# Optimization experiments

Measured on AMD Instinct MI355X. Metric: run time of the kernel, lower is better.

The kernel has to match this reference:

```python
import jax, jax.numpy as jnp
import numpy as np

N_NODES = 50000
N_EDGES = 1_600_000
IN_DIM = 128
OUT_DIM = 32
HEADS = 4
EDGE_DIM = 16


def setup_inputs() -> dict:
    key = jax.random.key(0)
    ks = jax.random.split(key, 8)
    x = jax.random.normal(ks[0], (N_NODES, IN_DIM), dtype=jnp.float32)
    edge_index = jax.random.randint(ks[1], (2, N_EDGES), 0, N_NODES, dtype=jnp.int32)
    edge_attr = jax.random.normal(ks[2], (N_EDGES, EDGE_DIM), dtype=jnp.float32)
    # parameters (xavier-ish small scale)
    W_lin = jax.random.normal(ks[3], (OUT_DIM * HEADS, IN_DIM), dtype=jnp.float32) * 0.08
    att_src = jax.random.normal(ks[4], (HEADS, OUT_DIM), dtype=jnp.float32) * 0.1
    att_dst = jax.random.normal(ks[5], (HEADS, OUT_DIM), dtype=jnp.float32) * 0.1
    bias = jnp.zeros((OUT_DIM,), dtype=jnp.float32)
    W_edge = jax.random.normal(ks[6], (HEADS, EDGE_DIM), dtype=jnp.float32) * 0.2
    return {"x": x, "edge_index": edge_index, "edge_attr": edge_attr,
            "W_lin": W_lin, "att_src": att_src, "att_dst": att_dst,
            "bias": bias, "W_edge": W_edge}


def reference(x, edge_index, edge_attr, W_lin, att_src, att_dst, bias, W_edge):
    num_nodes = x.shape[0]
    heads, out_dim = att_src.shape
    # h = lin(x) -> [N, H, D]
    h = (x @ W_lin.T).reshape(num_nodes, heads, out_dim)
    # per-node attention terms [N, H]
    a_src = jnp.einsum("nhd,hd->nh", h, att_src)
    a_dst = jnp.einsum("nhd,hd->nh", h, att_dst)
    src, dst = edge_index[0], edge_index[1]
    # edge logits [E, H]
    logits = a_src[src] + a_dst[dst] + edge_attr @ W_edge.T
    logits = jax.nn.leaky_relu(logits, negative_slope=0.2)
    # segment softmax over edges grouped by dst (vectorized across heads)
    max_vals = jax.ops.segment_max(logits, dst, num_segments=num_nodes)  # [N, H]
    exp_s = jnp.exp(logits - max_vals[dst])
    denom = jax.ops.segment_sum(exp_s, dst, num_segments=num_nodes)  # [N, H]
    alpha = exp_s / (denom[dst] + 1e-16)  # [E, H]
    # weighted aggregation: sum_e h[src_e] * alpha_e into dst nodes
    out = h[src] * alpha[:, :, None]  # [E, H, D]
    agg = jax.ops.segment_sum(out, dst, num_segments=num_nodes)  # [N, H, D]
    return agg.mean(axis=1) + bias
```

## Files before the change

### kernel.cpp

```cpp
#include <hip/hip_runtime.h>
#include <hip/hip_fp16.h>

#define N_NODES 50000
#define N_EDGES 1600000
#define IN_DIM  128
#define OUT_DIM 32
#define HEADS   4
#define EDGE_DIM 16

#define NB   512
#define DPB  98
#define CAP  4224
#define SC_CHUNK 1024
#define SC_EPT   4
#define PAD_DL 255

__global__ __launch_bounds__(256) void k_gemm(
    const float* __restrict__ x, const float* __restrict__ Wl,
    const float* __restrict__ att_src, const float* __restrict__ att_dst,
    __half* __restrict__ h2t, float* __restrict__ a_src,
    float* __restrict__ a_dst) {
  __shared__ float Wt[IN_DIM][68];
  __shared__ float xs[32][132];
  __shared__ float attS[IN_DIM], attD[IN_DIM];
  __shared__ float sred_s[32][4], sred_d[32][4];
  const int t = threadIdx.x;
  const int n0 = blockIdx.x * 32;

  if (t < IN_DIM) { attS[t] = att_src[t]; attD[t] = att_dst[t]; }

  for (int it = 0; it < 16; ++it) {
    int idx = it * 256 + t;
    int node = idx >> 7, i = idx & 127;
    int n = n0 + node;
    xs[node][i] = (n < N_NODES) ? x[(size_t)n * IN_DIM + i] : 0.f;
  }

  const int tx = t & 15, ty = t >> 4;
  const int na = n0 + 2 * ty, nb = na + 1;

  for (int p = 0; p < 2; ++p) {
    __syncthreads();
    for (int it = 0; it < 32; ++it) {
      int idx = it * 256 + t;
      int kg = (idx >> 7) + p * 64, i = idx & 127;
      Wt[i][kg - p * 64] = Wl[(size_t)kg * IN_DIM + i];
    }
    __syncthreads();

    float4 acc0 = {0.f,0.f,0.f,0.f}, acc1 = {0.f,0.f,0.f,0.f};
    for (int i4 = 0; i4 < IN_DIM; i4 += 4) {
      float4 xa = *(const float4*)&xs[2*ty][i4];
      float4 xb = *(const float4*)&xs[2*ty+1][i4];
      const float* xap = (const float*)&xa;
      const float* xbp = (const float*)&xb;
      #pragma unroll
      for (int ii = 0; ii < 4; ++ii) {
        float4 wv = *(const float4*)&Wt[i4+ii][tx*4];
        float a = xap[ii], b = xbp[ii];
        acc0.x += a*wv.x; acc0.y += a*wv.y; acc0.z += a*wv.z; acc0.w += a*wv.w;
        acc1.x += b*wv.x; acc1.y += b*wv.y; acc1.z += b*wv.z; acc1.w += b*wv.w;
      }
    }
    const int k = p*64 + tx*4;
    const int hd = k >> 5, d0 = k & 31;
    const float* ap = (const float*)&acc0;
    const float* bp = (const float*)&acc1;

    float sa = ap[0]*attS[k] + ap[1]*attS[k+1] + ap[2]*attS[k+2] + ap[3]*attS[k+3];
    float da = ap[0]*attD[k] + ap[1]*attD[k+1] + ap[2]*attD[k+2] + ap[3]*attD[k+3];
    float sb = bp[0]*attS[k] + bp[1]*attS[k+1] + bp[2]*attS[k+2] + bp[3]*attS[k+3];
    float db = bp[0]*attD[k] + bp[1]*attD[k+1] + bp[2]*attD[k+2] + bp[3]*attD[k+3];
    #pragma unroll
    for (int off = 1; off <= 4; off <<= 1) {
      sa += __shfl_xor(sa, off); da += __shfl_xor(da, off);
      sb += __shfl_xor(sb, off); db += __shfl_xor(db, off);
    }
    if ((tx & 7) == 0) {
      sred_s[2*ty][hd] = sa; sred_s[2*ty+1][hd] = sb;
      sred_d[2*ty][hd] = da; sred_d[2*ty+1][hd] = db;
    }

    if (na < N_NODES) {
      #pragma unroll
      for (int j = 0; j < 4; ++j)
        h2t[(size_t)na*IN_DIM + (d0+j)*4 + hd] = __float2half(ap[j]);
    }
    if (nb < N_NODES) {
      #pragma unroll
      for (int j = 0; j < 4; ++j)
        h2t[(size_t)nb*IN_DIM + (d0+j)*4 + hd] = __float2half(bp[j]);
    }
  }
  __syncthreads();
  if (t < 128) {
    int node = t >> 2;
    if (n0 + node < N_NODES)
      a_src[(size_t)(n0 + node) * 4 + (t & 3)] = sred_s[node][t & 3];
  } else {
    int tt = t - 128, node = tt >> 2;
    if (n0 + node < N_NODES)
      a_dst[(size_t)(n0 + node) * 4 + (tt & 3)] = sred_d[node][tt & 3];
  }
}

__global__ __launch_bounds__(256) void k_scatter3(
    const int* __restrict__ ei, const float* __restrict__ eattr,
    const float* __restrict__ a_src, const float* __restrict__ a_dst,
    const float* __restrict__ W_edge, unsigned int* __restrict__ gcursor,
    float4* __restrict__ rec) {
  __shared__ float We[HEADS * EDGE_DIM];
  __shared__ unsigned int cntb[NB], gbase[NB];
  const int t = threadIdx.x;
  if (t < HEADS * EDGE_DIM) We[t] = W_edge[t];
  for (int i = t; i < NB; i += 256) cntb[i] = 0u;
  __syncthreads();

  const int base = blockIdx.x * SC_CHUNK;
  unsigned int rx[SC_EPT], ry[SC_EPT], rz[SC_EPT], rk[SC_EPT];
  int bk[SC_EPT]; unsigned char dl8[SC_EPT]; bool ok[SC_EPT];

  #pragma unroll
  for (int i = 0; i < SC_EPT; ++i) {
    int e = base + i * 256 + t;
    ok[i] = (e < N_EDGES);
    if (ok[i]) {
      int src = ei[e], dst = ei[N_EDGES + e];
      float asp[4], adp[4], ea[EDGE_DIM];
      *(float4*)asp = *(const float4*)(a_src + (size_t)src * 4);
      *(float4*)adp = *(const float4*)(a_dst + (size_t)dst * 4);
      #pragma unroll
      for (int j = 0; j < 4; ++j)
        *(float4*)&ea[j*4] = *(const float4*)(eattr + (size_t)e * EDGE_DIM + j*4);
      float pv[HEADS];
      #pragma unroll
      for (int hh = 0; hh < HEADS; ++hh) {
        float sum = asp[hh] + adp[hh];
        #pragma unroll
        for (int j = 0; j < EDGE_DIM; ++j) sum += ea[j] * We[hh*EDGE_DIM + j];
        float lg = (sum > 0.f) ? sum : 0.2f * sum;
        pv[hh] = __expf(lg);
      }
      __half2 p01 = __floats2half2_rn(pv[0], pv[1]);
      __half2 p23 = __floats2half2_rn(pv[2], pv[3]);
      int b = dst / DPB;
      bk[i] = b;
      dl8[i] = (unsigned char)(dst - b * DPB);
      rx[i] = *(const unsigned int*)&p01;
      ry[i] = *(const unsigned int*)&p23;
      rz[i] = (unsigned int)src;
      rk[i] = atomicAdd(&cntb[b], 1u);
    }
  }
  __syncthreads();

  for (int b = t; b < NB; b += 256) {
    unsigned int c = cntb[b];
    if (c) {
      unsigned int creq = (c + 1u) & ~1u;
      unsigned int gb = atomicAdd(&gcursor[b], creq);
      gbase[b] = gb;
      if ((c & 1u) && (gb + c < CAP)) {
        float4 z;
        z.x = 0.f; z.y = 0.f; z.z = 0.f;
        z.w = __uint_as_float((unsigned int)PAD_DL);
        rec[(size_t)b * CAP + gb + c] = z;
      }
    }
  }
  __syncthreads();

  #pragma unroll
  for (int i = 0; i < SC_EPT; ++i) {
    if (ok[i]) {
      unsigned int pos = gbase[bk[i]] + rk[i];
      if (pos < CAP) {
        float4 r;
        r.x = __uint_as_float(rx[i]); r.y = __uint_as_float(ry[i]);
        r.z = __uint_as_float(rz[i]); r.w = __uint_as_float((unsigned int)dl8[i]);
        rec[(size_t)bk[i] * CAP + pos] = r;
      }
    }
  }
}

__global__ __launch_bounds__(1024) void k_bagg(
    const unsigned int* __restrict__ gcursor, const float4* __restrict__ rec,
    const __half* __restrict__ h2t, const float* __restrict__ bias,
    float* __restrict__ out) {
  __shared__ float4 srec[CAP];
  __shared__ unsigned short idx[CAP];
  __shared__ unsigned int cnt[256], off[256], cnt2[256];
  const int t = threadIdx.x;
  const int b = blockIdx.x;
  const size_t base = (size_t)b * CAP;
  unsigned int cntT = gcursor[b];
  if (cntT > CAP) cntT = CAP;

  if (t < 256) { cnt[t] = 0u; cnt2[t] = 0u; }
  __syncthreads();

  int dl_r[5]; unsigned short jj[5]; int nmine = 0;
  for (unsigned int j = t; j < cntT; j += 1024) {
    float4 r = rec[base + j];
    srec[j] = r;
    int dl = (int)__float_as_uint(r.w);
    dl_r[nmine] = dl; jj[nmine] = (unsigned short)j; ++nmine;
    atomicAdd(&cnt[dl], 1u);
  }
  __syncthreads();
  if (t == 0) {
    unsigned int run = 0;
    for (int i = 0; i < 256; ++i) { off[i] = run; run += cnt[i]; }
  }
  __syncthreads();
  for (int k = 0; k < nmine; ++k) {
    int dl = dl_r[k];
    if (dl != PAD_DL) {
      unsigned int r = atomicAdd(&cnt2[dl], 1u);
      idx[off[dl] + r] = jj[k];
    }
  }
  __syncthreads();

  const int wv = t >> 6, lane = t & 63, half_ = lane >> 5, dd = lane & 31;
  for (int dl = wv; dl < DPB; dl += 16) {
    int node = b * DPB + dl;
    if (node >= N_NODES) break;
    const unsigned int s0 = off[dl], c = cnt[dl];

    float acc0 = 0.f, acc1 = 0.f, acc2 = 0.f, acc3 = 0.f;
    float dn0 = 0.f, dn1 = 0.f, dn2 = 0.f, dn3 = 0.f;

    unsigned int j = half_;
    for (; j + 2 < c; j += 4) {
      float4 ra = srec[idx[s0 + j]];
      float4 rb = srec[idx[s0 + j + 2]];
      unsigned int a01 = __float_as_uint(ra.x), a23 = __float_as_uint(ra.y);
      unsigned int b01 = __float_as_uint(rb.x), b23 = __float_as_uint(rb.y);
      int sa = (int)__float_as_uint(ra.z), sb = (int)__float_as_uint(rb.z);
      uint2 hra = *(const uint2*)(h2t + (size_t)sa * IN_DIM + dd * 4);
      uint2 hrb = *(const uint2*)(h2t + (size_t)sb * IN_DIM + dd * 4);
      float2 pa01 = __half22float2(*(const __half2*)&a01);
      float2 pa23 = __half22float2(*(const __half2*)&a23);
      dn0 += pa01.x; dn1 += pa01.y; dn2 += pa23.x; dn3 += pa23.y;
      float2 ha01 = __half22float2(*(const __half2*)&hra.x);
      float2 ha23 = __half22float2(*(const __half2*)&hra.y);
      acc0 += pa01.x * ha01.x; acc1 += pa01.y * ha01.y;
      acc2 += pa23.x * ha23.x; acc3 += pa23.y * ha23.y;
      float2 pb01 = __half22float2(*(const __half2*)&b01);
      float2 pb23 = __half22float2(*(const __half2*)&b23);
      dn0 += pb01.x; dn1 += pb01.y; dn2 += pb23.x; dn3 += pb23.y;
      float2 hb01 = __half22float2(*(const __half2*)&hrb.x);
      float2 hb23 = __half22float2(*(const __half2*)&hrb.y);
      acc0 += pb01.x * hb01.x; acc1 += pb01.y * hb01.y;
      acc2 += pb23.x * hb23.x; acc3 += pb23.y * hb23.y;
    }
    for (; j < c; j += 2) {
      float4 r = srec[idx[s0 + j]];
      unsigned int u01 = __float_as_uint(r.x), u23 = __float_as_uint(r.y);
      int src = (int)__float_as_uint(r.z);
      uint2 raw = *(const uint2*)(h2t + (size_t)src * IN_DIM + dd * 4);
      float2 p01 = __half22float2(*(const __half2*)&u01);
      float2 p23 = __half22float2(*(const __half2*)&u23);
      dn0 += p01.x; dn1 += p01.y; dn2 += p23.x; dn3 += p23.y;
      float2 h01 = __half22float2(*(const __half2*)&raw.x);
      float2 h23 = __half22float2(*(const __half2*)&raw.y);
      acc0 += p01.x * h01.x; acc1 += p01.y * h01.y;
      acc2 += p23.x * h23.x; acc3 += p23.y * h23.y;
    }

    dn0 += __shfl_xor(dn0, 32); dn1 += __shfl_xor(dn1, 32);
    dn2 += __shfl_xor(dn2, 32); dn3 += __shfl_xor(dn3, 32);
    acc0 += __shfl_xor(acc0, 32); acc1 += __shfl_xor(acc1, 32);
    acc2 += __shfl_xor(acc2, 32); acc3 += __shfl_xor(acc3, 32);

    if (half_ == 0) {
      float v = acc0 * (0.25f / (dn0 + 1e-16f)) + acc1 * (0.25f / (dn1 + 1e-16f))
              + acc2 * (0.25f / (dn2 + 1e-16f)) + acc3 * (0.25f / (dn3 + 1e-16f));
      out[(size_t)node * OUT_DIM + dd] = v + bias[dd];
    }
  }
}

extern "C" void kernel_launch(void* const* d_in, const int* in_sizes, int n_in,
                              void* d_out, int out_size, void* d_ws, size_t ws_size,
                              hipStream_t stream) {
  const float* x       = (const float*)d_in[0];
  const int*   ei      = (const int*)d_in[1];
  const float* eattr   = (const float*)d_in[2];
  const float* W_lin   = (const float*)d_in[3];
  const float* att_src = (const float*)d_in[4];
  const float* att_dst = (const float*)d_in[5];
  const float* bias    = (const float*)d_in[6];
  const float* W_edge  = (const float*)d_in[7];
  float* out = (float*)d_out;

  __half* h2t  = (__half*)d_ws;
  float4* rec  = (float4*)(h2t + (size_t)N_NODES * IN_DIM);
  float* a_src = (float*)(rec + (size_t)NB * CAP);
  float* a_dst = a_src + (size_t)N_NODES * HEADS;
  unsigned int* gcursor = (unsigned int*)(a_dst + (size_t)N_NODES * HEADS);

  hipMemsetAsync(gcursor, 0, NB * sizeof(unsigned int), stream);

  k_gemm<<<(N_NODES + 31) / 32, 256, 0, stream>>>(
      x, W_lin, att_src, att_dst, h2t, a_src, a_dst);
  k_scatter3<<<(N_EDGES + SC_CHUNK - 1) / SC_CHUNK, 256, 0, stream>>>(
      ei, eattr, a_src, a_dst, W_edge, gcursor, rec);
  k_bagg<<<NB, 1024, 0, stream>>>(gcursor, rec, h2t, bias, out);
}
```

Measured before the change: 163.1 us.

## Read x directly in GEMM, defer edge logit math, pad cursor atomics

```diff
diff --git a/kernel.cpp b/kernel.cpp
--- a/kernel.cpp
+++ b/kernel.cpp
@@ -14,6 +14,7 @@
 #define SC_CHUNK 1024
 #define SC_EPT   4
 #define PAD_DL 255
+#define GC(b) ((b) * 16)
 
 __global__ __launch_bounds__(256) void k_gemm(
     const float* __restrict__ x, const float* __restrict__ Wl,
@@ -21,7 +22,6 @@
     __half* __restrict__ h2t, float* __restrict__ a_src,
     float* __restrict__ a_dst) {
   __shared__ float Wt[IN_DIM][68];
-  __shared__ float xs[32][132];
   __shared__ float attS[IN_DIM], attD[IN_DIM];
   __shared__ float sred_s[32][4], sred_d[32][4];
   const int t = threadIdx.x;
@@ -29,15 +29,10 @@
 
   if (t < IN_DIM) { attS[t] = att_src[t]; attD[t] = att_dst[t]; }
 
-  for (int it = 0; it < 16; ++it) {
-    int idx = it * 256 + t;
-    int node = idx >> 7, i = idx & 127;
-    int n = n0 + node;
-    xs[node][i] = (n < N_NODES) ? x[(size_t)n * IN_DIM + i] : 0.f;
-  }
-
   const int tx = t & 15, ty = t >> 4;
   const int na = n0 + 2 * ty, nb = na + 1;
+  const float* xa_ptr = x + (size_t)((na < N_NODES) ? na : 0) * IN_DIM;
+  const float* xb_ptr = x + (size_t)((nb < N_NODES) ? nb : 0) * IN_DIM;
 
   for (int p = 0; p < 2; ++p) {
     __syncthreads();
@@ -49,9 +44,10 @@
     __syncthreads();
 
     float4 acc0 = {0.f,0.f,0.f,0.f}, acc1 = {0.f,0.f,0.f,0.f};
+    #pragma unroll 4
     for (int i4 = 0; i4 < IN_DIM; i4 += 4) {
-      float4 xa = *(const float4*)&xs[2*ty][i4];
-      float4 xb = *(const float4*)&xs[2*ty+1][i4];
+      float4 xa = *(const float4*)(xa_ptr + i4);
+      float4 xb = *(const float4*)(xb_ptr + i4);
       const float* xap = (const float*)&xa;
       const float* xbp = (const float*)&xb;
       #pragma unroll
@@ -117,7 +113,7 @@
   __syncthreads();
 
   const int base = blockIdx.x * SC_CHUNK;
-  unsigned int rx[SC_EPT], ry[SC_EPT], rz[SC_EPT], rk[SC_EPT];
+  unsigned int rk[SC_EPT];
   int bk[SC_EPT]; unsigned char dl8[SC_EPT]; bool ok[SC_EPT];
 
   #pragma unroll
@@ -125,30 +121,10 @@
     int e = base + i * 256 + t;
     ok[i] = (e < N_EDGES);
     if (ok[i]) {
-      int src = ei[e], dst = ei[N_EDGES + e];
-      float asp[4], adp[4], ea[EDGE_DIM];
-      *(float4*)asp = *(const float4*)(a_src + (size_t)src * 4);
-      *(float4*)adp = *(const float4*)(a_dst + (size_t)dst * 4);
-      #pragma unroll
-      for (int j = 0; j < 4; ++j)
-        *(float4*)&ea[j*4] = *(const float4*)(eattr + (size_t)e * EDGE_DIM + j*4);
-      float pv[HEADS];
-      #pragma unroll
-      for (int hh = 0; hh < HEADS; ++hh) {
-        float sum = asp[hh] + adp[hh];
-        #pragma unroll
-        for (int j = 0; j < EDGE_DIM; ++j) sum += ea[j] * We[hh*EDGE_DIM + j];
-        float lg = (sum > 0.f) ? sum : 0.2f * sum;
-        pv[hh] = __expf(lg);
-      }
-      __half2 p01 = __floats2half2_rn(pv[0], pv[1]);
-      __half2 p23 = __floats2half2_rn(pv[2], pv[3]);
+      int dst = ei[N_EDGES + e];
       int b = dst / DPB;
       bk[i] = b;
       dl8[i] = (unsigned char)(dst - b * DPB);
-      rx[i] = *(const unsigned int*)&p01;
-      ry[i] = *(const unsigned int*)&p23;
-      rz[i] = (unsigned int)src;
       rk[i] = atomicAdd(&cntb[b], 1u);
     }
   }
@@ -158,7 +134,7 @@
     unsigned int c = cntb[b];
     if (c) {
       unsigned int creq = (c + 1u) & ~1u;
-      unsigned int gb = atomicAdd(&gcursor[b], creq);
+      unsigned int gb = atomicAdd(&gcursor[GC(b)], creq);
       gbase[b] = gb;
       if ((c & 1u) && (gb + c < CAP)) {
         float4 z;
@@ -172,14 +148,37 @@
 
   #pragma unroll
   for (int i = 0; i < SC_EPT; ++i) {
-    if (ok[i]) {
-      unsigned int pos = gbase[bk[i]] + rk[i];
-      if (pos < CAP) {
-        float4 r;
-        r.x = __uint_as_float(rx[i]); r.y = __uint_as_float(ry[i]);
-        r.z = __uint_as_float(rz[i]); r.w = __uint_as_float((unsigned int)dl8[i]);
-        rec[(size_t)bk[i] * CAP + pos] = r;
-      }
+    if (!ok[i]) continue;
+    int e = base + i * 256 + t;
+    int src = ei[e];
+    float asp[4], adp[4], ea[EDGE_DIM];
+    *(float4*)asp = *(const float4*)(a_src + (size_t)src * 4);
+    {
+      int dst = bk[i] * DPB + (int)dl8[i];
+      *(float4*)adp = *(const float4*)(a_dst + (size_t)dst * 4);
+    }
+    #pragma unroll
+    for (int j = 0; j < 4; ++j)
+      *(float4*)&ea[j*4] = *(const float4*)(eattr + (size_t)e * EDGE_DIM + j*4);
+    float pv[HEADS];
+    #pragma unroll
+    for (int hh = 0; hh < HEADS; ++hh) {
+      float sum = asp[hh] + adp[hh];
+      #pragma unroll
+      for (int j = 0; j < EDGE_DIM; ++j) sum += ea[j] * We[hh*EDGE_DIM + j];
+      float lg = (sum > 0.f) ? sum : 0.2f * sum;
+      pv[hh] = __expf(lg);
+    }
+    __half2 p01 = __floats2half2_rn(pv[0], pv[1]);
+    __half2 p23 = __floats2half2_rn(pv[2], pv[3]);
+    unsigned int pos = gbase[bk[i]] + rk[i];
+    if (pos < CAP) {
+      float4 r;
+      r.x = __uint_as_float(*(const unsigned int*)&p01);
+      r.y = __uint_as_float(*(const unsigned int*)&p23);
+      r.z = __uint_as_float((unsigned int)src);
+      r.w = __uint_as_float((unsigned int)dl8[i]);
+      rec[(size_t)bk[i] * CAP + pos] = r;
     }
   }
 }
@@ -194,7 +193,7 @@
   const int t = threadIdx.x;
   const int b = blockIdx.x;
   const size_t base = (size_t)b * CAP;
-  unsigned int cntT = gcursor[b];
+  unsigned int cntT = gcursor[GC(b)];
   if (cntT > CAP) cntT = CAP;
 
   if (t < 256) { cnt[t] = 0u; cnt2[t] = 0u; }
@@ -302,7 +301,7 @@
   float* a_dst = a_src + (size_t)N_NODES * HEADS;
   unsigned int* gcursor = (unsigned int*)(a_dst + (size_t)N_NODES * HEADS);
 
-  hipMemsetAsync(gcursor, 0, NB * sizeof(unsigned int), stream);
+  hipMemsetAsync(gcursor, 0, (size_t)NB * 16 * sizeof(unsigned int), stream);
 
   k_gemm<<<(N_NODES + 31) / 32, 256, 0, stream>>>(
       x, W_lin, att_src, att_dst, h2t, a_src, a_dst);
```

Result: slower. 198.4 us (+21.7%).
